# Performance work log

Measured on AMD Instinct MI355X. Metric: run time of the kernel, lower is better.

The kernel has to match this reference:

```python
import jax, jax.numpy as jnp
import numpy as np

B, T, D, H = 4, 1024, 1024, 16


def setup_inputs() -> dict:
    key = jax.random.key(0)
    ks = jax.random.split(key, 8)
    s = 0.02
    return {
        "query": jax.random.normal(ks[0], (B, T, D), jnp.float32),
        "key": jax.random.normal(ks[1], (B, T, D), jnp.float32),
        "values": jax.random.normal(ks[2], (B, T, D), jnp.float32),
        "Wq": jax.random.normal(ks[3], (D, D), jnp.float32) * s,
        "bq": jnp.zeros((D,), jnp.float32),
        "Wv": jax.random.normal(ks[4], (D, D), jnp.float32) * s,
        "bv": jnp.zeros((D,), jnp.float32),
        "Wo": jax.random.normal(ks[5], (D, D), jnp.float32) * s,
        "bo": jnp.zeros((D,), jnp.float32),
        "gammas": jax.random.normal(ks[6], (H,), jnp.float32) * 0.1,
        "ln_g": jnp.ones((D,), jnp.float32),
        "ln_b": jnp.zeros((D,), jnp.float32),
    }


def _layer(query, key, values, Wq, bq, Wv, bv, Wo, bo, gammas, ln_g, ln_b):
    b, t, d = query.shape
    h = gammas.shape[0]
    dk = d // h

    def proj(x, W, bias):  # torch Linear: x @ W.T + b, then split heads -> (b,h,t,dk)
        y = jnp.einsum('btd,ed->bte', x, W) + bias
        return y.reshape(b, t, h, dk).transpose(0, 2, 1, 3)

    q = proj(query, Wq, bq)
    k = proj(key, Wq, bq)   # kq_same=True
    v = proj(values, Wv, bv)

    scores = jnp.einsum('bhqd,bhkd->bhqk', q, k) / np.float32(np.sqrt(dk))
    idx = jnp.arange(t)
    pos = jnp.abs(idx[:, None] - idx[None, :]).astype(scores.dtype)  # |i-j|, (t,t)
    mask = idx[:, None] > idx[None, :]  # strict lower tril (peek_cur=False)
    neg = jnp.asarray(-1e32, scores.dtype)

    # gamma time-effect (computed without grad in original)
    s_ = jax.nn.softmax(jnp.where(mask, scores, neg), axis=-1)
    distcum = jnp.cumsum(s_, axis=-1)
    disttotal = jnp.sum(s_, axis=-1, keepdims=True)
    dist = jnp.sqrt(jnp.clip((disttotal - distcum) * pos, 0.0, None))
    dist = jax.lax.stop_gradient(dist)
    gamma_eff = -jnp.abs(gammas)[None, :, None, None]  # (1,h,1,1)
    total_effect = jnp.clip(jnp.exp(dist * gamma_eff), 1e-5, 1e5)
    scores = scores * total_effect

    p = jax.nn.softmax(jnp.where(mask, scores, neg), axis=-1)
    p = jnp.where(mask, p, 0.0)
    # maxout rescale (maxout=True since peek_cur=False)
    scale = jnp.minimum(1.0 / jnp.max(p, axis=-1, keepdims=True), 5.0)
    p = p * scale

    out = jnp.einsum('bhqk,bhkd->bhqd', p, v)
    concat = out.transpose(0, 2, 1, 3).reshape(b, t, d)
    attn_out = jnp.einsum('btd,ed->bte', concat, Wo) + bo

    x = query + attn_out  # residual (dropout is identity in eval)
    mu = jnp.mean(x, axis=-1, keepdims=True)
    var = jnp.var(x, axis=-1, keepdims=True)
    return (x - mu) / jnp.sqrt(var + 1e-5) * ln_g + ln_b


def reference(query, key, values, Wq, bq, Wv, bv, Wo, bo, gammas, ln_g, ln_b):
    return _layer(query, key, values, Wq, bq, Wv, bv, Wo, bo, gammas, ln_g, ln_b)
```

## Files before the change

### kernel.cpp

```cpp
#include <hip/hip_runtime.h>
#include <hip/hip_bf16.h>
#include <stdint.h>


typedef unsigned short ushort_t;
typedef __attribute__((ext_vector_type(8))) short short8;
typedef __attribute__((ext_vector_type(8))) unsigned short u16x8;
typedef __attribute__((ext_vector_type(4))) float f32x4;
typedef __attribute__((ext_vector_type(4))) unsigned short u16x4;
typedef __attribute__((ext_vector_type(2))) unsigned short u16x2;

#define GLB_CAST(p) ((const __attribute__((address_space(1))) void*)(p))
#define LDS_CAST(p) ((__attribute__((address_space(3))) void*)(p))

#if __has_builtin(__builtin_amdgcn_exp2f)
#define EXP2F(x) __builtin_amdgcn_exp2f(x)
#else
#define EXP2F(x) exp2f(x)
#endif

#define LOG2E 1.44269504f

__device__ __forceinline__ float b2f(ushort_t u) {
  union { unsigned int i; float f; } x; x.i = ((unsigned int)u) << 16; return x.f;
}
__device__ __forceinline__ ushort_t f2b(float f) {
  __hip_bfloat16 h = __float2bfloat16(f);
  return *reinterpret_cast<ushort_t*>(&h);
}
__device__ __forceinline__ float wave_sum(float v) {
  #pragma unroll
  for (int d = 32; d > 0; d >>= 1) v += __shfl_xor(v, d);
  return v;
}

__global__ void conv6_f32_bf16(const float* __restrict__ s0, const float* __restrict__ s1,
                               const float* __restrict__ s2, const float* __restrict__ s3,
                               const float* __restrict__ s4, const float* __restrict__ s5,
                               ushort_t* __restrict__ d0, ushort_t* __restrict__ d1,
                               ushort_t* __restrict__ d2, ushort_t* __restrict__ d3,
                               ushort_t* __restrict__ d4, ushort_t* __restrict__ d5,
                               int n4tok, int n4w) {
  const int y = blockIdx.y;
  const float* srcs[6] = {s0, s1, s2, s3, s4, s5};
  ushort_t*    dsts[6] = {d0, d1, d2, d3, d4, d5};
  const int n4 = (y < 3) ? n4tok : n4w;
  int i = blockIdx.x * blockDim.x + threadIdx.x;
  if (i < n4) {
    const float4 v = reinterpret_cast<const float4*>(srcs[y])[i];
    u16x4 o;
    o[0] = f2b(v.x); o[1] = f2b(v.y); o[2] = f2b(v.z); o[3] = f2b(v.w);
    reinterpret_cast<u16x4*>(dsts[y])[i] = o;
  }
}

__device__ __forceinline__ void gemm_core(const ushort_t* __restrict__ A,
                                          const ushort_t* __restrict__ Bt,
                                          int m0, int n0,
                                          ushort_t* As, ushort_t* Bs,
                                          f32x4 (&acc)[4][4]) {
  const int tid = threadIdx.x, lane = tid & 63;
  const int wid = tid >> 6;
  const int wr = (wid >> 1) * 64, wc = (wid & 1) * 64;
  for (int k0 = 0; k0 < 1024; k0 += 32) {
    #pragma unroll
    for (int it = 0; it < 2; ++it) {
      const int idx = tid * 8 + it * 2048;
      const int r = idx >> 5, kk = idx & 31;
      __builtin_amdgcn_global_load_lds(GLB_CAST(&A[(size_t)(m0 + r) * 1024 + k0 + kk]),
                                       LDS_CAST(&As[idx]), 16, 0, 0);
      __builtin_amdgcn_global_load_lds(GLB_CAST(&Bt[(size_t)(n0 + r) * 1024 + k0 + kk]),
                                       LDS_CAST(&Bs[idx]), 16, 0, 0);
    }
    __syncthreads();
    short8 af[4], bfv[4];
    #pragma unroll
    for (int m = 0; m < 4; ++m)
      af[m] = *reinterpret_cast<const short8*>(&As[(wr + m * 16 + (lane & 15)) * 32 + (lane >> 4) * 8]);
    #pragma unroll
    for (int n = 0; n < 4; ++n)
      bfv[n] = *reinterpret_cast<const short8*>(&Bs[(wc + n * 16 + (lane & 15)) * 32 + (lane >> 4) * 8]);
    #pragma unroll
    for (int m = 0; m < 4; ++m)
      #pragma unroll
      for (int n = 0; n < 4; ++n)
        acc[m][n] = __builtin_amdgcn_mfma_f32_16x16x32_bf16(af[m], bfv[n], acc[m][n], 0, 0, 0);
    __syncthreads();
  }
}

__global__ __launch_bounds__(256) void gemm_proj(
    const ushort_t* __restrict__ qb, const ushort_t* __restrict__ kb, const ushort_t* __restrict__ vb,
    const ushort_t* __restrict__ Wqb, const ushort_t* __restrict__ Wvb,
    const float* __restrict__ bq, const float* __restrict__ bvv,
    ushort_t* __restrict__ Qh, ushort_t* __restrict__ Kh, ushort_t* __restrict__ Vt) {
  __shared__ ushort_t As[128 * 32], Bs[128 * 32];
  const ushort_t* A; const ushort_t* Bt; const float* bias;
  if (blockIdx.z == 0)      { A = qb; Bt = Wqb; bias = bq;  }
  else if (blockIdx.z == 1) { A = kb; Bt = Wqb; bias = bq;  }
  else                      { A = vb; Bt = Wvb; bias = bvv; }
  const int m0 = blockIdx.y * 128, n0 = blockIdx.x * 128;
  f32x4 zero = {0.f, 0.f, 0.f, 0.f};
  f32x4 acc[4][4];
  #pragma unroll
  for (int m = 0; m < 4; ++m)
    #pragma unroll
    for (int n = 0; n < 4; ++n) acc[m][n] = zero;
  gemm_core(A, Bt, m0, n0, As, Bs, acc);
  const int lane = threadIdx.x & 63, wid = threadIdx.x >> 6;
  const int wr = (wid >> 1) * 64, wc = (wid & 1) * 64;
  if (blockIdx.z == 2) {
    #pragma unroll
    for (int m = 0; m < 4; ++m)
      #pragma unroll
      for (int n = 0; n < 4; ++n) {
        const int rowb = m0 + wr + m * 16 + (lane >> 4) * 4;
        const int col  = n0 + wc + n * 16 + (lane & 15);
        u16x4 pk;
        #pragma unroll
        for (int r4 = 0; r4 < 4; ++r4) pk[r4] = f2b(acc[m][n][r4] + bias[col]);
        const int bi = rowb >> 10, t = rowb & 1023;
        *reinterpret_cast<u16x4*>(
            &Vt[((size_t)(bi * 16 + (col >> 6)) * 64 + (col & 63)) * 1024 + t]) = pk;
      }
  } else {
    ushort_t* dst = (blockIdx.z == 0) ? Qh : Kh;
    #pragma unroll
    for (int m = 0; m < 4; ++m)
      #pragma unroll
      for (int n = 0; n < 4; ++n)
        #pragma unroll
        for (int r4 = 0; r4 < 4; ++r4) {
          const int row = m0 + wr + m * 16 + (lane >> 4) * 4 + r4;
          const int col = n0 + wc + n * 16 + (lane & 15);
          const float v = acc[m][n][r4] + bias[col];
          const int bi = row >> 10, t = row & 1023, h = col >> 6, dd = col & 63;
          dst[((size_t)(bi * 16 + h) * 1024 + t) * 64 + dd] = f2b(v);
        }
  }
}

__global__ __launch_bounds__(256) void gemm_out(
    const ushort_t* __restrict__ A, const ushort_t* __restrict__ Bt,
    const float* __restrict__ bias, const float* __restrict__ resid,
    ushort_t* __restrict__ dstB) {
  __shared__ ushort_t As[128 * 32], Bs[128 * 32];
  const int m0 = blockIdx.y * 128, n0 = blockIdx.x * 128;
  f32x4 zero = {0.f, 0.f, 0.f, 0.f};
  f32x4 acc[4][4];
  #pragma unroll
  for (int m = 0; m < 4; ++m)
    #pragma unroll
    for (int n = 0; n < 4; ++n) acc[m][n] = zero;
  gemm_core(A, Bt, m0, n0, As, Bs, acc);
  const int lane = threadIdx.x & 63, wid = threadIdx.x >> 6;
  const int wr = (wid >> 1) * 64, wc = (wid & 1) * 64;
  #pragma unroll
  for (int m = 0; m < 4; ++m)
    #pragma unroll
    for (int n = 0; n < 4; ++n)
      #pragma unroll
      for (int r4 = 0; r4 < 4; ++r4) {
        const int row = m0 + wr + m * 16 + (lane >> 4) * 4 + r4;
        const int col = n0 + wc + n * 16 + (lane & 15);
        const size_t o = (size_t)row * 1024 + col;
        dstB[o] = f2b(acc[m][n][r4] + bias[col] + resid[o]);
      }
}

template<int CH>
__device__ __forceinline__ void load_row(const ushort_t* __restrict__ Row, float (&s)[CH]) {
  constexpr int W = (CH % 8 == 0) ? 8 : (CH % 4 == 0) ? 4 : (CH % 2 == 0) ? 2 : 1;
  #pragma unroll
  for (int b = 0; b < CH / W; ++b) {
    if constexpr (W == 8) {
      const u16x8 t = *reinterpret_cast<const u16x8*>(&Row[b * 8]);
      #pragma unroll
      for (int e = 0; e < 8; ++e) s[b * 8 + e] = b2f(t[e]);
    } else if constexpr (W == 4) {
      const u16x4 t = *reinterpret_cast<const u16x4*>(&Row[b * 4]);
      #pragma unroll
      for (int e = 0; e < 4; ++e) s[b * 4 + e] = b2f(t[e]);
    } else if constexpr (W == 2) {
      const u16x2 t = *reinterpret_cast<const u16x2*>(&Row[b * 2]);
      s[b * 2] = b2f(t[0]); s[b * 2 + 1] = b2f(t[1]);
    } else {
      s[b] = b2f(Row[b]);
    }
  }
}

template<int CH>
__device__ __forceinline__ void store_row(ushort_t* __restrict__ Row,
                                          const float (&p)[CH], const float sc) {
  constexpr int W = (CH % 8 == 0) ? 8 : (CH % 4 == 0) ? 4 : (CH % 2 == 0) ? 2 : 1;
  #pragma unroll
  for (int b = 0; b < CH / W; ++b) {
    if constexpr (W == 8) {
      u16x8 o;
      #pragma unroll
      for (int e = 0; e < 8; ++e) o[e] = f2b(p[b * 8 + e] * sc);
      *reinterpret_cast<u16x8*>(&Row[b * 8]) = o;
    } else if constexpr (W == 4) {
      u16x4 o;
      #pragma unroll
      for (int e = 0; e < 4; ++e) o[e] = f2b(p[b * 4 + e] * sc);
      *reinterpret_cast<u16x4*>(&Row[b * 4]) = o;
    } else if constexpr (W == 2) {
      u16x2 o;
      o[0] = f2b(p[b * 2] * sc); o[1] = f2b(p[b * 2 + 1] * sc);
      *reinterpret_cast<u16x2*>(&Row[b * 2]) = o;
    } else {
      Row[b] = f2b(p[b] * sc);
    }
  }
}

template<int CH>
__device__ __forceinline__ void phase_b(ushort_t* __restrict__ Sb, const int i0,
                                        const int w, const int lane, const float gamx) {
  const int c0 = CH * lane;
  for (int rr = 0; rr < 4; ++rr) {
    const int r = w * 4 + rr;
    const int i = i0 + r;
    ushort_t* __restrict__ Row = &Sb[r * 1032 + c0];
    if (i == 0) {
      #pragma unroll
      for (int e = 0; e < CH; ++e) Row[e] = 0;
      continue;
    }
    const int nact = min(max(i - c0, 0), CH);
    float s[CH], ev[CH];
    load_row<CH>(Row, s);
    float run = 0.f;
    #pragma unroll
    for (int e = 0; e < CH; ++e) {
      s[e] = (e < nact) ? s[e] : -__builtin_inff();
      ev[e] = EXP2F(s[e]);
      run += ev[e];
    }
    float v = run;
    #pragma unroll
    for (int d = 1; d < 64; d <<= 1) {
      const float t = __shfl_down(v, d);
      v += (lane + d < 64) ? t : 0.f;
    }
    const float Z1 = __shfl(v, 0);
    float run2 = v - run;
    const float g2 = -gamx * rsqrtf(Z1);
    const float posb = (float)(i - c0);
    float z2 = 0.f, mm = 0.f;
    #pragma unroll
    for (int e = CH - 1; e >= 0; --e) {
      const float t = fmaxf(run2 * (posb - (float)e), 0.f);
      run2 += ev[e];
      const float eff = fmaxf(EXP2F(g2 * sqrtf(t)), 1e-5f);
      const float p = EXP2F(s[e] * eff);
      ev[e] = p;
      z2 += p;
      mm = fmaxf(mm, p);
    }
    #pragma unroll
    for (int d = 32; d > 0; d >>= 1) {
      z2 += __shfl_xor(z2, d);
      mm = fmaxf(mm, __shfl_xor(mm, d));
    }
    const float sc = fminf(1.f / mm, 5.f / z2);
    store_row<CH>(Row, ev, sc);
  }
}

__global__ __launch_bounds__(256, 4) void attn_kernel(
    const ushort_t* __restrict__ Qh, const ushort_t* __restrict__ Kh,
    const ushort_t* __restrict__ Vt, const float* __restrict__ gammas,
    ushort_t* __restrict__ concat) {
  __shared__ __align__(16) ushort_t Sb[16 * 1032];
  __shared__ __align__(16) ushort_t Qs[16 * 72];
  const int tid = threadIdx.x, lane = tid & 63, w = tid >> 6;
  const int flat = blockIdx.x + (blockIdx.y << 6);
  const int bh = ((flat & 7) << 3) | (flat >> 9);
  const int i0 = (63 - ((flat >> 3) & 63)) << 4;
  const int bi = bh >> 4, h = bh & 15;
  const size_t base = (size_t)bh * (1024 * 64);

  {
    const int r = tid >> 4, d = (tid & 15) * 4;
    *reinterpret_cast<u16x4*>(&Qs[r * 72 + d]) =
        *reinterpret_cast<const u16x4*>(&Qh[base + (size_t)(i0 + r) * 64 + d]);
  }
  __syncthreads();

  const int upper = i0 + 16;
  for (int nt = 0; nt < 16; ++nt) {
    const int colbase = (nt * 4 + w) * 16;
    if (colbase >= upper) break;
    f32x4 acc = {0.f, 0.f, 0.f, 0.f};
    #pragma unroll
    for (int kt = 0; kt < 2; ++kt) {
      const short8 a = *reinterpret_cast<const short8*>(
          &Qs[(lane & 15) * 72 + kt * 32 + (lane >> 4) * 8]);
      const short8 bb = *reinterpret_cast<const short8*>(
          &Kh[base + (size_t)(colbase + (lane & 15)) * 64 + kt * 32 + (lane >> 4) * 8]);
      acc = __builtin_amdgcn_mfma_f32_16x16x32_bf16(a, bb, acc, 0, 0, 0);
    }
    const int j = colbase + (lane & 15);
    #pragma unroll
    for (int r4 = 0; r4 < 4; ++r4) {
      const int rf = (lane >> 4) * 4 + r4;
      Sb[rf * 1032 + j] = f2b(acc[r4] * (0.125f * LOG2E));
    }
  }
  __syncthreads();

  const float gamx = fabsf(gammas[h]) * LOG2E;
  const int chp = (upper + 63) >> 6;
  switch (chp) {
    case 1:           phase_b<1 >(Sb, i0, w, lane, gamx); break;
    case 2:           phase_b<2 >(Sb, i0, w, lane, gamx); break;
    case 3: case 4:   phase_b<4 >(Sb, i0, w, lane, gamx); break;
    case 5: case 6:   phase_b<6 >(Sb, i0, w, lane, gamx); break;
    case 7: case 8:   phase_b<8 >(Sb, i0, w, lane, gamx); break;
    case 9: case 10:  phase_b<10>(Sb, i0, w, lane, gamx); break;
    case 11: case 12: phase_b<12>(Sb, i0, w, lane, gamx); break;
    case 13: case 14: phase_b<14>(Sb, i0, w, lane, gamx); break;
    default:          phase_b<16>(Sb, i0, w, lane, gamx); break;
  }
  __syncthreads();

  {
    const int d0 = w * 16;
    const int arow = lane & 15;
    const ushort_t* Prow = &Sb[arow * 1032];
    const ushort_t* Vrow = Vt + base + (size_t)(d0 + arow) * 1024;
    const int kmax = (upper + 31) & ~31;
    f32x4 acc = {0.f, 0.f, 0.f, 0.f};
    for (int k0 = 0; k0 < kmax; k0 += 32) {
      const short8 a = *reinterpret_cast<const short8*>(&Prow[k0 + (lane >> 4) * 8]);
      const short8 bb = *reinterpret_cast<const short8*>(&Vrow[k0 + (lane >> 4) * 8]);
      acc = __builtin_amdgcn_mfma_f32_16x16x32_bf16(a, bb, acc, 0, 0, 0);
    }
    #pragma unroll
    for (int r4 = 0; r4 < 4; ++r4) {
      const int row = (lane >> 4) * 4 + r4;
      const int i = i0 + row;
      concat[((size_t)(bi * 1024 + i)) * 1024 + h * 64 + d0 + arow] = f2b(acc[r4]);
    }
  }
}

__global__ __launch_bounds__(256) void ln_kernel(const ushort_t* __restrict__ x,
                                                 const float* __restrict__ g,
                                                 const float* __restrict__ bb,
                                                 float* __restrict__ out) {
  const int row = blockIdx.x, tid = threadIdx.x, lane = tid & 63, w = tid >> 6;
  const u16x4 xv = reinterpret_cast<const u16x4*>(x + (size_t)row * 1024)[tid];
  float v0 = b2f(xv[0]), v1 = b2f(xv[1]), v2 = b2f(xv[2]), v3 = b2f(xv[3]);
  float s = v0 + v1 + v2 + v3;
  float q = v0 * v0 + v1 * v1 + v2 * v2 + v3 * v3;
  s = wave_sum(s); q = wave_sum(q);
  __shared__ float ps[4], pq[4];
  if (lane == 0) { ps[w] = s; pq[w] = q; }
  __syncthreads();
  const float ts = ps[0] + ps[1] + ps[2] + ps[3];
  const float tq = pq[0] + pq[1] + pq[2] + pq[3];
  const float mu = ts * (1.f / 1024.f);
  const float inv = rsqrtf(tq * (1.f / 1024.f) - mu * mu + 1e-5f);
  const float4 gv = reinterpret_cast<const float4*>(g)[tid];
  const float4 bv = reinterpret_cast<const float4*>(bb)[tid];
  float4 o;
  o.x = (v0 - mu) * inv * gv.x + bv.x;
  o.y = (v1 - mu) * inv * gv.y + bv.y;
  o.z = (v2 - mu) * inv * gv.z + bv.z;
  o.w = (v3 - mu) * inv * gv.w + bv.w;
  reinterpret_cast<float4*>(out + (size_t)row * 1024)[tid] = o;
}

extern "C" void kernel_launch(void* const* d_in, const int* in_sizes, int n_in,
                              void* d_out, int out_size, void* d_ws, size_t ws_size,
                              hipStream_t stream) {
  (void)in_sizes; (void)n_in; (void)out_size; (void)ws_size;
  const float* query  = (const float*)d_in[0];
  const float* key    = (const float*)d_in[1];
  const float* values = (const float*)d_in[2];
  const float* Wq     = (const float*)d_in[3];
  const float* bq     = (const float*)d_in[4];
  const float* Wv     = (const float*)d_in[5];
  const float* bv     = (const float*)d_in[6];
  const float* Wo     = (const float*)d_in[7];
  const float* bo     = (const float*)d_in[8];
  const float* gammas = (const float*)d_in[9];
  const float* ln_g   = (const float*)d_in[10];
  const float* ln_b   = (const float*)d_in[11];
  float* out = (float*)d_out;

  const size_t NT = 4096ull * 1024;
  const size_t NW = 1024ull * 1024;
  char* p = (char*)d_ws;
  ushort_t* qb  = (ushort_t*)p; p += NT * 2;
  ushort_t* kb  = (ushort_t*)p; p += NT * 2;
  ushort_t* vb  = (ushort_t*)p; p += NT * 2;
  ushort_t* Wqb = (ushort_t*)p; p += NW * 2;
  ushort_t* Wvb = (ushort_t*)p; p += NW * 2;
  ushort_t* Wob = (ushort_t*)p; p += NW * 2;
  ushort_t* Qh  = (ushort_t*)p; p += NT * 2;
  ushort_t* Kh  = (ushort_t*)p; p += NT * 2;
  ushort_t* Vt  = (ushort_t*)p; p += NT * 2;
  ushort_t* concat = vb;
  ushort_t* xbuf   = qb;

  conv6_f32_bf16<<<dim3(4096, 6), 256, 0, stream>>>(
      query, key, values, Wq, Wv, Wo, qb, kb, vb, Wqb, Wvb, Wob,
      (int)(NT / 4), (int)(NW / 4));

  gemm_proj<<<dim3(8, 32, 3), 256, 0, stream>>>(qb, kb, vb, Wqb, Wvb, bq, bv, Qh, Kh, Vt);
  attn_kernel<<<dim3(64, 64), 256, 0, stream>>>(Qh, Kh, Vt, gammas, concat);
  gemm_out<<<dim3(8, 32), 256, 0, stream>>>(concat, Wob, bo, query, xbuf);
  ln_kernel<<<4096, 256, 0, stream>>>(xbuf, ln_g, ln_b, out);
}
```

Before: 171.8 us.

## Split attention kernel into long-row and short-row launches with smaller LDS

The single causal attention launch is replaced by two templated launches. One handles the upper half of query tiles with the full 1032-wide score buffer. The other handles the lower half with a 520-wide LDS buffer and a higher minimum-waves launch bound, so short rows get more occupancy and fewer phase_b specializations. The cost is an extra kernel launch and a serialization point between the two halves, which may leave the tail of the first launch underfilled.

```diff
diff --git a/kernel.cpp b/kernel.cpp
--- a/kernel.cpp
+++ b/kernel.cpp
@@ -216,14 +216,14 @@
   }
 }
 
-template<int CH>
+template<int CH, int SROW>
 __device__ __forceinline__ void phase_b(ushort_t* __restrict__ Sb, const int i0,
                                         const int w, const int lane, const float gamx) {
   const int c0 = CH * lane;
   for (int rr = 0; rr < 4; ++rr) {
     const int r = w * 4 + rr;
     const int i = i0 + r;
-    ushort_t* __restrict__ Row = &Sb[r * 1032 + c0];
+    ushort_t* __restrict__ Row = &Sb[r * SROW + c0];
     if (i == 0) {
       #pragma unroll
       for (int e = 0; e < CH; ++e) Row[e] = 0;
@@ -270,16 +270,17 @@
   }
 }
 
-__global__ __launch_bounds__(256, 4) void attn_kernel(
+template<int SROW, int NTMAX, int TILEREV, int MINW>
+__global__ __launch_bounds__(256, MINW) void attn_kernel_t(
     const ushort_t* __restrict__ Qh, const ushort_t* __restrict__ Kh,
     const ushort_t* __restrict__ Vt, const float* __restrict__ gammas,
     ushort_t* __restrict__ concat) {
-  __shared__ __align__(16) ushort_t Sb[16 * 1032];
+  __shared__ __align__(16) ushort_t Sb[16 * SROW];
   __shared__ __align__(16) ushort_t Qs[16 * 72];
   const int tid = threadIdx.x, lane = tid & 63, w = tid >> 6;
-  const int flat = blockIdx.x + (blockIdx.y << 6);
-  const int bh = ((flat & 7) << 3) | (flat >> 9);
-  const int i0 = (63 - ((flat >> 3) & 63)) << 4;
+  const int flat = blockIdx.x;
+  const int bh = ((flat & 7) << 3) | (flat >> 8);
+  const int i0 = (TILEREV - ((flat >> 3) & 31)) << 4;
   const int bi = bh >> 4, h = bh & 15;
   const size_t base = (size_t)bh * (1024 * 64);
 
@@ -291,7 +292,7 @@
   __syncthreads();
 
   const int upper = i0 + 16;
-  for (int nt = 0; nt < 16; ++nt) {
+  for (int nt = 0; nt < NTMAX; ++nt) {
     const int colbase = (nt * 4 + w) * 16;
     if (colbase >= upper) break;
     f32x4 acc = {0.f, 0.f, 0.f, 0.f};
@@ -307,30 +308,35 @@
     #pragma unroll
     for (int r4 = 0; r4 < 4; ++r4) {
       const int rf = (lane >> 4) * 4 + r4;
-      Sb[rf * 1032 + j] = f2b(acc[r4] * (0.125f * LOG2E));
+      Sb[rf * SROW + j] = f2b(acc[r4] * (0.125f * LOG2E));
     }
   }
   __syncthreads();
 
   const float gamx = fabsf(gammas[h]) * LOG2E;
   const int chp = (upper + 63) >> 6;
-  switch (chp) {
-    case 1:           phase_b<1 >(Sb, i0, w, lane, gamx); break;
-    case 2:           phase_b<2 >(Sb, i0, w, lane, gamx); break;
-    case 3: case 4:   phase_b<4 >(Sb, i0, w, lane, gamx); break;
-    case 5: case 6:   phase_b<6 >(Sb, i0, w, lane, gamx); break;
-    case 7: case 8:   phase_b<8 >(Sb, i0, w, lane, gamx); break;
-    case 9: case 10:  phase_b<10>(Sb, i0, w, lane, gamx); break;
-    case 11: case 12: phase_b<12>(Sb, i0, w, lane, gamx); break;
-    case 13: case 14: phase_b<14>(Sb, i0, w, lane, gamx); break;
-    default:          phase_b<16>(Sb, i0, w, lane, gamx); break;
+  if constexpr (NTMAX == 8) {
+    switch (chp) {
+      case 1:         phase_b<1, SROW>(Sb, i0, w, lane, gamx); break;
+      case 2:         phase_b<2, SROW>(Sb, i0, w, lane, gamx); break;
+      case 3: case 4: phase_b<4, SROW>(Sb, i0, w, lane, gamx); break;
+      case 5: case 6: phase_b<6, SROW>(Sb, i0, w, lane, gamx); break;
+      default:        phase_b<8, SROW>(Sb, i0, w, lane, gamx); break;
+    }
+  } else {
+    switch (chp) {
+      case 9:  case 10: phase_b<10, SROW>(Sb, i0, w, lane, gamx); break;
+      case 11: case 12: phase_b<12, SROW>(Sb, i0, w, lane, gamx); break;
+      case 13: case 14: phase_b<14, SROW>(Sb, i0, w, lane, gamx); break;
+      default:          phase_b<16, SROW>(Sb, i0, w, lane, gamx); break;
+    }
   }
   __syncthreads();
 
   {
     const int d0 = w * 16;
     const int arow = lane & 15;
-    const ushort_t* Prow = &Sb[arow * 1032];
+    const ushort_t* Prow = &Sb[arow * SROW];
     const ushort_t* Vrow = Vt + base + (size_t)(d0 + arow) * 1024;
     const int kmax = (upper + 31) & ~31;
     f32x4 acc = {0.f, 0.f, 0.f, 0.f};
@@ -413,7 +419,8 @@
       (int)(NT / 4), (int)(NW / 4));
 
   gemm_proj<<<dim3(8, 32, 3), 256, 0, stream>>>(qb, kb, vb, Wqb, Wvb, bq, bv, Qh, Kh, Vt);
-  attn_kernel<<<dim3(64, 64), 256, 0, stream>>>(Qh, Kh, Vt, gammas, concat);
+  attn_kernel_t<1032, 16, 63, 4><<<dim3(2048), 256, 0, stream>>>(Qh, Kh, Vt, gammas, concat);
+  attn_kernel_t<520,  8,  31, 8><<<dim3(2048), 256, 0, stream>>>(Qh, Kh, Vt, gammas, concat);
   gemm_out<<<dim3(8, 32), 256, 0, stream>>>(concat, Wob, bo, query, xbuf);
   ln_kernel<<<4096, 256, 0, stream>>>(xbuf, ln_g, ln_b, out);
 }
```

Result: slower. 185.2 us (+7.8%).
